# Kernel optimization log

Hardware: AMD Instinct MI355X
Metric: run time of the kernel (lower is better)

## Reference

```python
import jax, jax.numpy as jnp
import numpy as np

N = 100000
IN_C = 128
HID = 16
HEADS = 8
OUT_C = 64
E = 1600000
NEG_SLOPE = 0.2
EPS = 1e-16


def setup_inputs() -> dict:
    key = jax.random.key(0)
    ks = jax.random.split(key, 12)
    s = lambda k, shape, fan: jax.random.normal(k, shape, jnp.float32) * (1.0 / np.sqrt(fan))
    return {
        "x": jax.random.normal(ks[0], (N, IN_C), jnp.float32),
        "edge_index": jax.random.randint(ks[1], (2, E), 0, N, jnp.int64),
        # conv1 params (heads=8, concat=True)
        "W1": s(ks[2], (IN_C, HEADS * HID), IN_C),
        "a_src1": s(ks[3], (HEADS, HID), HID),
        "a_dst1": s(ks[4], (HEADS, HID), HID),
        "b1": jnp.zeros((HEADS * HID,), jnp.float32),
        # conv2 params (heads=1, concat=False)
        "W2": s(ks[5], (HEADS * HID, OUT_C), HEADS * HID),
        "a_src2": s(ks[6], (1, OUT_C), OUT_C),
        "a_dst2": s(ks[7], (1, OUT_C), OUT_C),
        "b2": jnp.zeros((OUT_C,), jnp.float32),
    }


def gat_conv(x, src, dst, W, a_src, a_dst, bias, concat):
    """PyG-style GATConv: edge softmax over incoming edges + scatter-add."""
    H, C = a_src.shape
    n = x.shape[0]
    h = (x @ W).reshape(n, H, C)                      # [N,H,C]
    asrc = jnp.einsum("nhc,hc->nh", h, a_src)          # [N,H]
    adst = jnp.einsum("nhc,hc->nh", h, a_dst)          # [N,H]
    e = jax.nn.leaky_relu(asrc[src] + adst[dst], NEG_SLOPE)  # [E,H]
    # numerically-stable segment softmax over edges sharing a destination
    m = jax.ops.segment_max(e, dst, num_segments=n)    # [N,H]
    m = jnp.where(jnp.isfinite(m), m, 0.0)
    ex = jnp.exp(e - m[dst])                           # [E,H]
    denom = jax.ops.segment_sum(ex, dst, num_segments=n)  # [N,H]
    alpha = ex / (denom[dst] + EPS)                    # [E,H]
    out = jax.ops.segment_sum(alpha[:, :, None] * h[src], dst, num_segments=n)  # [N,H,C]
    out = out.reshape(n, H * C) if concat else out.mean(axis=1)
    return out + bias


def reference(x, edge_index, W1, a_src1, a_dst1, b1, W2, a_src2, a_dst2, b2):
    n = x.shape[0]
    # PyG GATConv adds self-loops by default
    loop = jnp.arange(n, dtype=edge_index.dtype)
    src = jnp.concatenate([edge_index[0], loop])
    dst = jnp.concatenate([edge_index[1], loop])
    # dropout(p=0.6) is identity at inference
    h = jax.nn.elu(gat_conv(x, src, dst, W1, a_src1, a_dst1, b1, concat=True))
    return gat_conv(h, src, dst, W2, a_src2, a_dst2, b2, concat=False)
```

## Files before the change

kernel.cpp:

```cpp
#include <hip/hip_runtime.h>
#include <hip/hip_bf16.h>
#include <math.h>


typedef __attribute__((ext_vector_type(8))) short short8;
typedef __attribute__((ext_vector_type(4))) float f32x4;

__device__ __forceinline__ float bflo(uint u) { return __uint_as_float(u << 16); }
__device__ __forceinline__ float bfhi(uint u) { return __uint_as_float(u & 0xffff0000u); }
__device__ __forceinline__ float bf1(ushort v) { return __uint_as_float(((uint)v) << 16); }
__device__ __forceinline__ ushort f2bf(float f) {
    uint u = __float_as_uint(f);
    u += 0x7fff + ((u >> 16) & 1);
    return (ushort)(u >> 16);
}
#define LOG2E 1.44269504088896f

#define CSR_CAP 4096

__global__ __launch_bounds__(512) void k_bhist(const int* __restrict__ dst, int e,
                                               int* __restrict__ bcount) {
    __shared__ int h[1024];
    int t = threadIdx.x;
    for (int i = t; i < 1024; i += 512) h[i] = 0;
    __syncthreads();
    int c0 = blockIdx.x * 8192, c1 = min(c0 + 8192, e);
    for (int i = c0 + t; i < c1; i += 512) atomicAdd(&h[dst[i] >> 7], 1);
    __syncthreads();
    for (int i = t; i < 1024; i += 512)
        if (h[i]) atomicAdd(&bcount[i], h[i]);
}

__global__ __launch_bounds__(256) void k_bscan(const int* __restrict__ bcount, int nb, int n,
                                               int* __restrict__ ebase, int* __restrict__ ecur,
                                               int* __restrict__ cbase) {
    __shared__ int ae[1024], be[1024], ac[1024], bc[1024];
    int t = threadIdx.x;
    for (int i = t; i < 1024; i += 256) {
        int v = 0, nn = 0;
        if (i < nb) {
            v = bcount[i];
            nn = min(128, n - (i << 7));
        }
        ae[i] = v;
        ac[i] = v + nn;
    }
    __syncthreads();
    int* pa = ae; int* qa = be; int* pc = ac; int* qc = bc;
    for (int off = 1; off < 1024; off <<= 1) {
        for (int i = t; i < 1024; i += 256) {
            int va = pa[i], vc = pc[i];
            if (i >= off) { va += pa[i - off]; vc += pc[i - off]; }
            qa[i] = va; qc[i] = vc;
        }
        __syncthreads();
        int* tm = pa; pa = qa; qa = tm;
        tm = pc; pc = qc; qc = tm;
    }
    for (int i = t; i < 1024; i += 256) {
        if (i < nb) {
            int ea = (i == 0) ? 0 : pa[i - 1];
            int ca = (i == 0) ? 0 : pc[i - 1];
            ebase[i] = ea; ecur[i] = ea; cbase[i] = ca;
        }
    }
}

__global__ __launch_bounds__(512) void k_part(const int* __restrict__ src,
                                              const int* __restrict__ dst, int e,
                                              int* __restrict__ ecur, int* __restrict__ ebuf) {
    __shared__ int h[1024];
    __shared__ int base[1024];
    int t = threadIdx.x;
    int c0 = blockIdx.x * 8192, c1 = min(c0 + 8192, e);
    for (int i = t; i < 1024; i += 512) h[i] = 0;
    __syncthreads();
    for (int i = c0 + t; i < c1; i += 512) atomicAdd(&h[dst[i] >> 7], 1);
    __syncthreads();
    for (int i = t; i < 1024; i += 512) {
        int c = h[i];
        base[i] = c ? atomicAdd(&ecur[i], c) : 0;
        h[i] = 0;
    }
    __syncthreads();
    for (int i = c0 + t; i < c1; i += 512) {
        int d = dst[i], b = d >> 7;
        int r = atomicAdd(&h[b], 1);
        ebuf[base[b] + r] = (src[i] << 7) | (d & 127);
    }
}

__global__ __launch_bounds__(256) void k_build(const int* __restrict__ ebuf,
                                               const int* __restrict__ bcount,
                                               const int* __restrict__ ebase,
                                               const int* __restrict__ cbase,
                                               int* __restrict__ rowptr,
                                               int* __restrict__ csr, int n, int nb) {
    __shared__ int cnt[128];
    __shared__ int sc[128], sc2[128];
    __shared__ int csr_l[CSR_CAP];
    int b = blockIdx.x, t = threadIdx.x;
    int n0 = b << 7;
    int nn = min(128, n - n0);
    int ec = bcount[b], eb = ebase[b], cb = cbase[b];
    if (t < 128) cnt[t] = 0;
    __syncthreads();
    for (int i = t; i < ec; i += 256) atomicAdd(&cnt[ebuf[eb + i] & 127], 1);
    __syncthreads();
    if (t < 128) sc[t] = (t < nn) ? cnt[t] + 1 : 0;
    __syncthreads();
    int* p = sc; int* q = sc2;
    for (int off = 1; off < 128; off <<= 1) {
        if (t < 128) {
            int v = p[t];
            if (t >= off) v += p[t - off];
            q[t] = v;
        }
        __syncthreads();
        int* tm = p; p = q; q = tm;
    }
    int total = p[127];
    if (total <= CSR_CAP) {
        if (t < nn) {
            int off = (t == 0) ? 0 : p[t - 1];
            rowptr[n0 + t] = cb + off;
            csr_l[off] = n0 + t;
            cnt[t] = off + 1;
        }
        __syncthreads();
        for (int i = t; i < ec; i += 256) {
            int v = ebuf[eb + i];
            int s = atomicAdd(&cnt[v & 127], 1);
            csr_l[s] = v >> 7;
        }
        __syncthreads();
        for (int i = t; i < total; i += 256) csr[cb + i] = csr_l[i];
    } else {
        if (t < nn) {
            int off = (t == 0) ? 0 : p[t - 1];
            rowptr[n0 + t] = cb + off;
            csr[cb + off] = n0 + t;
            cnt[t] = off + 1;
        }
        __syncthreads();
        for (int i = t; i < ec; i += 256) {
            int v = ebuf[eb + i];
            int s = atomicAdd(&cnt[v & 127], 1);
            csr[cb + s] = v >> 7;
        }
    }
    if (b == nb - 1 && t == 0) rowptr[n] = cb + total;
}

template <int COLS, bool XBF16>
__global__ __launch_bounds__(256) void k_gemm_mfma(const void* __restrict__ Xv,
                                                   const float* __restrict__ W,
                                                   ushort* __restrict__ Y, int n) {
    __shared__ ushort As[128][136];
    __shared__ ushort Ws[COLS][136];
    const int t = threadIdx.x;
    const int row0 = blockIdx.x * 128;
    if constexpr (!XBF16) {
        const float* X = (const float*)Xv;
#pragma unroll
        for (int q = 0; q < 16; q++) {
            int idx = t + q * 256;
            int r = idx >> 5, c4 = (idx & 31) * 4;
            float4 xv = make_float4(0.f, 0.f, 0.f, 0.f);
            if (row0 + r < n) xv = *reinterpret_cast<const float4*>(&X[(size_t)(row0 + r) * 128 + c4]);
            ushort4 w4 = make_ushort4(f2bf(xv.x), f2bf(xv.y), f2bf(xv.z), f2bf(xv.w));
            *reinterpret_cast<ushort4*>(&As[r][c4]) = w4;
        }
    } else {
        const ushort* X = (const ushort*)Xv;
#pragma unroll
        for (int q = 0; q < 8; q++) {
            int idx = t + q * 256;
            int r = idx >> 4, c8 = (idx & 15) * 8;
            uint4 v = make_uint4(0u, 0u, 0u, 0u);
            if (row0 + r < n) v = *reinterpret_cast<const uint4*>(&X[(size_t)(row0 + r) * 128 + c8]);
            *reinterpret_cast<uint4*>(&As[r][c8]) = v;
        }
    }
    for (int i = t; i < 128 * COLS; i += 256) {
        int k = i / COLS, nc = i % COLS;
        Ws[nc][k] = f2bf(W[i]);
    }
    __syncthreads();
    const int w = t >> 6, l = t & 63;
    const int lr = l & 15;
    const int lk = (l >> 4) * 8;
    f32x4 acc[2][COLS / 16];
#pragma unroll
    for (int m = 0; m < 2; m++)
#pragma unroll
        for (int nb = 0; nb < COLS / 16; nb++) acc[m][nb] = (f32x4){0.f, 0.f, 0.f, 0.f};
#pragma unroll
    for (int kc = 0; kc < 128; kc += 32) {
        short8 a0 = *reinterpret_cast<const short8*>(&As[w * 32 + lr][kc + lk]);
        short8 a1 = *reinterpret_cast<const short8*>(&As[w * 32 + 16 + lr][kc + lk]);
#pragma unroll
        for (int nb = 0; nb < COLS / 16; nb++) {
            short8 bf = *reinterpret_cast<const short8*>(&Ws[nb * 16 + lr][kc + lk]);
            acc[0][nb] = __builtin_amdgcn_mfma_f32_16x16x32_bf16(a0, bf, acc[0][nb], 0, 0, 0);
            acc[1][nb] = __builtin_amdgcn_mfma_f32_16x16x32_bf16(a1, bf, acc[1][nb], 0, 0, 0);
        }
    }
#pragma unroll
    for (int m = 0; m < 2; m++)
#pragma unroll
        for (int j = 0; j < 4; j++) {
            int r = row0 + w * 32 + m * 16 + (l >> 4) * 4 + j;
            if (r < n) {
#pragma unroll
                for (int nb = 0; nb < COLS / 16; nb++)
                    Y[(size_t)r * COLS + nb * 16 + lr] = f2bf(acc[m][nb][j]);
            }
        }
}

__global__ void k_attn1(const uint* __restrict__ hu, const float* __restrict__ a_src,
                        const float* __restrict__ a_dst, float* __restrict__ asrc,
                        float* __restrict__ adst, int n) {
    int t = blockIdx.x * 256 + threadIdx.x;
    if (t >= n * 8) return;
    int node = t >> 3, hd = t & 7;
    const uint* hp = hu + (size_t)node * 64 + hd * 8;
    float s1 = 0.f, s2 = 0.f;
#pragma unroll
    for (int q = 0; q < 8; q++) {
        uint u = hp[q];
        float v0 = bflo(u), v1 = bfhi(u);
        s1 = fmaf(v0, a_src[hd * 16 + 2 * q], s1);
        s1 = fmaf(v1, a_src[hd * 16 + 2 * q + 1], s1);
        s2 = fmaf(v0, a_dst[hd * 16 + 2 * q], s2);
        s2 = fmaf(v1, a_dst[hd * 16 + 2 * q + 1], s2);
    }
    asrc[t] = s1 * LOG2E;
    adst[t] = s2 * LOG2E;
}
__global__ void k_attn2(const uint* __restrict__ hu, const float* __restrict__ a_src,
                        const float* __restrict__ a_dst, float* __restrict__ asrc,
                        float* __restrict__ adst, int n) {
    int t = blockIdx.x * 256 + threadIdx.x;
    if (t >= n * 8) return;
    int node = t >> 3, j = t & 7;
    const uint* hp = hu + (size_t)node * 32 + j * 4;
    float s1 = 0.f, s2 = 0.f;
#pragma unroll
    for (int q = 0; q < 4; q++) {
        uint u = hp[q];
        float v0 = bflo(u), v1 = bfhi(u);
        s1 = fmaf(v0, a_src[j * 8 + 2 * q], s1);
        s1 = fmaf(v1, a_src[j * 8 + 2 * q + 1], s1);
        s2 = fmaf(v0, a_dst[j * 8 + 2 * q], s2);
        s2 = fmaf(v1, a_dst[j * 8 + 2 * q + 1], s2);
    }
#pragma unroll
    for (int o = 1; o < 8; o <<= 1) {
        s1 += __shfl_xor(s1, o);
        s2 += __shfl_xor(s2, o);
    }
    if (j == 0) { asrc[node] = s1 * LOG2E; adst[node] = s2 * LOG2E; }
}

__global__ __launch_bounds__(256) void k_agg1(
    const uint* __restrict__ hu, const float* __restrict__ asrc,
    const float* __restrict__ adst, const int* __restrict__ rowptr,
    const int* __restrict__ csr, const float* __restrict__ b1,
    uint* __restrict__ x2, int n) {
    __shared__ float P[4][512];
    int wv = threadIdx.x >> 6;
    int wid = (blockIdx.x * 256 + threadIdx.x) >> 6;
    if (wid >= n) return;
    uint lane = threadIdx.x & 63;
    uint hd = lane >> 3;
    uint sl = lane & 7;
    uint c0 = lane * 2;
    float adn = adst[(uint)wid * 8u + hd];
    int beg = rowptr[wid], end = rowptr[wid + 1];
    float s = 0.f, acc0 = 0.f, acc1 = 0.f;
    for (int base = beg; base < end; base += 64) {
        int cnt = min(64, end - base);
        int vidx = ((int)lane < cnt) ? csr[base + lane] : 0;
#pragma unroll
        for (int m = 0; m < 8; m++) {
            int slot = 8 * m + (int)sl;
            int cs = csr[base + min(slot, cnt - 1)];
            float e = asrc[(uint)cs * 8u + hd] + adn;
            e = fmaxf(e, 0.2f * e);
            P[wv][slot * 8 + hd] = exp2f(e);
        }
        asm volatile("s_waitcnt lgkmcnt(0)" ::: "memory");
        int j = 0;
        for (; j + 8 <= cnt; j += 8) {
            uint s0 = __builtin_amdgcn_readlane(vidx, j);
            uint s1 = __builtin_amdgcn_readlane(vidx, j + 1);
            uint s2 = __builtin_amdgcn_readlane(vidx, j + 2);
            uint s3 = __builtin_amdgcn_readlane(vidx, j + 3);
            uint s4 = __builtin_amdgcn_readlane(vidx, j + 4);
            uint s5 = __builtin_amdgcn_readlane(vidx, j + 5);
            uint s6 = __builtin_amdgcn_readlane(vidx, j + 6);
            uint s7 = __builtin_amdgcn_readlane(vidx, j + 7);
            uint u0 = hu[s0 * 64u + lane];
            uint u1 = hu[s1 * 64u + lane];
            uint u2 = hu[s2 * 64u + lane];
            uint u3 = hu[s3 * 64u + lane];
            uint u4 = hu[s4 * 64u + lane];
            uint u5 = hu[s5 * 64u + lane];
            uint u6 = hu[s6 * 64u + lane];
            uint u7 = hu[s7 * 64u + lane];
            float q0 = P[wv][(j + 0) * 8 + hd];
            float q1 = P[wv][(j + 1) * 8 + hd];
            float q2 = P[wv][(j + 2) * 8 + hd];
            float q3 = P[wv][(j + 3) * 8 + hd];
            float q4 = P[wv][(j + 4) * 8 + hd];
            float q5 = P[wv][(j + 5) * 8 + hd];
            float q6 = P[wv][(j + 6) * 8 + hd];
            float q7 = P[wv][(j + 7) * 8 + hd];
            s += ((q0 + q1) + (q2 + q3)) + ((q4 + q5) + (q6 + q7));
            acc0 = fmaf(q0, bflo(u0), fmaf(q1, bflo(u1), acc0));
            acc0 = fmaf(q2, bflo(u2), fmaf(q3, bflo(u3), acc0));
            acc0 = fmaf(q4, bflo(u4), fmaf(q5, bflo(u5), acc0));
            acc0 = fmaf(q6, bflo(u6), fmaf(q7, bflo(u7), acc0));
            acc1 = fmaf(q0, bfhi(u0), fmaf(q1, bfhi(u1), acc1));
            acc1 = fmaf(q2, bfhi(u2), fmaf(q3, bfhi(u3), acc1));
            acc1 = fmaf(q4, bfhi(u4), fmaf(q5, bfhi(u5), acc1));
            acc1 = fmaf(q6, bfhi(u6), fmaf(q7, bfhi(u7), acc1));
        }
        for (; j < cnt; ++j) {
            uint s0 = __builtin_amdgcn_readlane(vidx, j);
            float q0 = P[wv][j * 8 + hd];
            uint u0 = hu[s0 * 64u + lane];
            s += q0;
            acc0 = fmaf(q0, bflo(u0), acc0);
            acc1 = fmaf(q0, bfhi(u0), acc1);
        }
    }
    float inv = 1.f / (s + 1e-16f);
    float o0 = acc0 * inv + b1[c0];
    float o1 = acc1 * inv + b1[c0 + 1];
    o0 = o0 > 0.f ? o0 : (__expf(o0) - 1.f);
    o1 = o1 > 0.f ? o1 : (__expf(o1) - 1.f);
    union { ushort b[2]; uint u; } pk;
    pk.b[0] = f2bf(o0);
    pk.b[1] = f2bf(o1);
    x2[(uint)wid * 64u + lane] = pk.u;
}
__global__ __launch_bounds__(256) void k_agg2(
    const ushort* __restrict__ hb, const float* __restrict__ asrc,
    const float* __restrict__ adst, const int* __restrict__ rowptr,
    const int* __restrict__ csr, const float* __restrict__ b2,
    float* __restrict__ out, int n) {
    __shared__ float P2[4][64];
    int wv = threadIdx.x >> 6;
    int wid = (blockIdx.x * 256 + threadIdx.x) >> 6;
    if (wid >= n) return;
    uint lane = threadIdx.x & 63;
    float adn = adst[wid];
    int beg = rowptr[wid], end = rowptr[wid + 1];
    float s = 0.f, acc = 0.f;
    for (int base = beg; base < end; base += 64) {
        int cnt = min(64, end - base);
        int vidx = csr[base + min((int)lane, cnt - 1)];
        float e = asrc[vidx] + adn;
        e = fmaxf(e, 0.2f * e);
        P2[wv][lane] = ((int)lane < cnt) ? exp2f(e) : 0.f;
        asm volatile("s_waitcnt lgkmcnt(0)" ::: "memory");
        int j = 0;
        for (; j + 8 <= cnt; j += 8) {
            uint s0 = __builtin_amdgcn_readlane(vidx, j);
            uint s1 = __builtin_amdgcn_readlane(vidx, j + 1);
            uint s2 = __builtin_amdgcn_readlane(vidx, j + 2);
            uint s3 = __builtin_amdgcn_readlane(vidx, j + 3);
            uint s4 = __builtin_amdgcn_readlane(vidx, j + 4);
            uint s5 = __builtin_amdgcn_readlane(vidx, j + 5);
            uint s6 = __builtin_amdgcn_readlane(vidx, j + 6);
            uint s7 = __builtin_amdgcn_readlane(vidx, j + 7);
            float h0 = bf1(hb[s0 * 64u + lane]);
            float h1 = bf1(hb[s1 * 64u + lane]);
            float h2 = bf1(hb[s2 * 64u + lane]);
            float h3 = bf1(hb[s3 * 64u + lane]);
            float h4 = bf1(hb[s4 * 64u + lane]);
            float h5 = bf1(hb[s5 * 64u + lane]);
            float h6 = bf1(hb[s6 * 64u + lane]);
            float h7 = bf1(hb[s7 * 64u + lane]);
            float q0 = P2[wv][j + 0];
            float q1 = P2[wv][j + 1];
            float q2 = P2[wv][j + 2];
            float q3 = P2[wv][j + 3];
            float q4 = P2[wv][j + 4];
            float q5 = P2[wv][j + 5];
            float q6 = P2[wv][j + 6];
            float q7 = P2[wv][j + 7];
            s += ((q0 + q1) + (q2 + q3)) + ((q4 + q5) + (q6 + q7));
            acc = fmaf(q0, h0, fmaf(q1, h1, acc));
            acc = fmaf(q2, h2, fmaf(q3, h3, acc));
            acc = fmaf(q4, h4, fmaf(q5, h5, acc));
            acc = fmaf(q6, h6, fmaf(q7, h7, acc));
        }
        for (; j < cnt; ++j) {
            uint s0 = __builtin_amdgcn_readlane(vidx, j);
            float q0 = P2[wv][j];
            float h0 = bf1(hb[s0 * 64u + lane]);
            s += q0;
            acc = fmaf(q0, h0, acc);
        }
    }
    out[(size_t)wid * 64 + lane] = acc / (s + 1e-16f) + b2[lane];
}

extern "C" void kernel_launch(void* const* d_in, const int* in_sizes, int n_in,
                              void* d_out, int out_size, void* d_ws, size_t ws_size,
                              hipStream_t stream) {
    const float* x   = (const float*)d_in[0];
    const int*   ei  = (const int*)d_in[1];
    const float* W1  = (const float*)d_in[2];
    const float* as1 = (const float*)d_in[3];
    const float* ad1 = (const float*)d_in[4];
    const float* b1  = (const float*)d_in[5];
    const float* W2  = (const float*)d_in[6];
    const float* as2 = (const float*)d_in[7];
    const float* ad2 = (const float*)d_in[8];
    const float* b2  = (const float*)d_in[9];
    float* out = (float*)d_out;

    int N = in_sizes[0] / 128;
    int E = in_sizes[1] / 2;
    int TOT = E + N;
    const int* src = ei;
    const int* dst = ei + E;

    char* p = (char*)d_ws;
    auto alloc = [&](size_t bytes) {
        char* r = p;
        p += (bytes + 255) & ~size_t(255);
        return r;
    };
    ushort* h1b  = (ushort*)alloc((size_t)N * 128 * 2);
    ushort* h2b  = (ushort*)alloc((size_t)N * 64 * 2);
    ushort* x2b  = (ushort*)alloc((size_t)N * 128 * 2);
    float* asrc1 = (float*)alloc((size_t)N * 8 * 4);
    float* adst1 = (float*)alloc((size_t)N * 8 * 4);
    float* asrc2 = (float*)alloc((size_t)N * 4);
    float* adst2 = (float*)alloc((size_t)N * 4);
    int* rowptr  = (int*)alloc((size_t)(N + 1) * 4);
    int* csr     = (int*)alloc((size_t)TOT * 4);
    int* ebuf    = (int*)alloc((size_t)E * 4);
    int* bcount  = (int*)alloc(1024 * 4);
    int* ebase   = (int*)alloc(1024 * 4);
    int* ecur    = (int*)alloc(1024 * 4);
    int* cbase   = (int*)alloc(1024 * 4);

    int NB = (N + 127) >> 7;
    int nbp = (E + 8191) / 8192;

    hipMemsetAsync(bcount, 0, 1024 * 4, stream);
    k_bhist<<<nbp, 512, 0, stream>>>(dst, E, bcount);
    k_bscan<<<1, 256, 0, stream>>>(bcount, NB, N, ebase, ecur, cbase);
    k_part<<<nbp, 512, 0, stream>>>(src, dst, E, ecur, ebuf);
    k_build<<<NB, 256, 0, stream>>>(ebuf, bcount, ebase, cbase, rowptr, csr, N, NB);

    int gb = (N + 127) / 128;
    k_gemm_mfma<128, false><<<gb, 256, 0, stream>>>(x, W1, h1b, N);
    k_attn1<<<(N * 8 + 255) / 256, 256, 0, stream>>>((const uint*)h1b, as1, ad1, asrc1, adst1, N);
    k_agg1<<<(N + 3) / 4, 256, 0, stream>>>((const uint*)h1b, asrc1, adst1, rowptr, csr, b1,
                                            (uint*)x2b, N);

    k_gemm_mfma<64, true><<<gb, 256, 0, stream>>>(x2b, W2, h2b, N);
    k_attn2<<<(N * 8 + 255) / 256, 256, 0, stream>>>((const uint*)h2b, as2, ad2, asrc2, adst2, N);
    k_agg2<<<(N + 3) / 4, 256, 0, stream>>>((const ushort*)h2b, asrc2, adst2, rowptr, csr, b2,
                                            out, N);
}
```

Measured before the change: 242.0 us.

## Fuse CSR histogram into first GEMM and bucket scan into attention-logit kernel

Merges the edge-destination histogram with the layer-1 GEMM into one launch, with block ranges split by blockIdx and shared memory unioned. It also merges the single-block bucket scan with the layer-1 attention-logit kernel. This cuts two kernel launches and lets independent preprocessing overlap with the dense work. The agg1 edge-logit loop now iterates only over the occupied groups of 8 slots instead of always 8, skipping exp work for short neighbour lists at the cost of loop overhead. The unioned shared memory is sized for the GEMM, so histogram blocks may get lower occupancy.

```diff
diff --git a/kernel.cpp b/kernel.cpp
--- a/kernel.cpp
+++ b/kernel.cpp
@@ -15,55 +15,129 @@
     return (ushort)(u >> 16);
 }
 #define LOG2E 1.44269504088896f
-
 #define CSR_CAP 4096
 
-__global__ __launch_bounds__(512) void k_bhist(const int* __restrict__ dst, int e,
-                                               int* __restrict__ bcount) {
-    __shared__ int h[1024];
-    int t = threadIdx.x;
-    for (int i = t; i < 1024; i += 512) h[i] = 0;
-    __syncthreads();
-    int c0 = blockIdx.x * 8192, c1 = min(c0 + 8192, e);
-    for (int i = c0 + t; i < c1; i += 512) atomicAdd(&h[dst[i] >> 7], 1);
-    __syncthreads();
-    for (int i = t; i < 1024; i += 512)
-        if (h[i]) atomicAdd(&bcount[i], h[i]);
-}
-
-__global__ __launch_bounds__(256) void k_bscan(const int* __restrict__ bcount, int nb, int n,
-                                               int* __restrict__ ebase, int* __restrict__ ecur,
-                                               int* __restrict__ cbase) {
+__global__ __launch_bounds__(256) void k_gemm1_bhist(
+    const float* __restrict__ X, const float* __restrict__ W,
+    ushort* __restrict__ Y, int n,
+    const int* __restrict__ dst, int e, int* __restrict__ bcount, int nbh) {
+    __shared__ union {
+        struct { ushort As[128][136]; ushort Ws[128][136]; } g;
+        int h[1024];
+    } sm;
+    const int t = threadIdx.x;
+    if ((int)blockIdx.x < nbh) {
+        for (int i = t; i < 1024; i += 256) sm.h[i] = 0;
+        __syncthreads();
+        int c0 = blockIdx.x * 8192, c1 = min(c0 + 8192, e);
+        for (int i = c0 + t; i < c1; i += 256) atomicAdd(&sm.h[dst[i] >> 7], 1);
+        __syncthreads();
+        for (int i = t; i < 1024; i += 256)
+            if (sm.h[i]) atomicAdd(&bcount[i], sm.h[i]);
+        return;
+    }
+    const int row0 = (blockIdx.x - nbh) * 128;
+#pragma unroll
+    for (int q = 0; q < 16; q++) {
+        int idx = t + q * 256;
+        int r = idx >> 5, c4 = (idx & 31) * 4;
+        float4 xv = make_float4(0.f, 0.f, 0.f, 0.f);
+        if (row0 + r < n) xv = *reinterpret_cast<const float4*>(&X[(size_t)(row0 + r) * 128 + c4]);
+        ushort4 w4 = make_ushort4(f2bf(xv.x), f2bf(xv.y), f2bf(xv.z), f2bf(xv.w));
+        *reinterpret_cast<ushort4*>(&sm.g.As[r][c4]) = w4;
+    }
+    for (int i = t; i < 128 * 128; i += 256) {
+        int k = i >> 7, nc = i & 127;
+        sm.g.Ws[nc][k] = f2bf(W[i]);
+    }
+    __syncthreads();
+    const int w = t >> 6, l = t & 63;
+    const int lr = l & 15;
+    const int lk = (l >> 4) * 8;
+    f32x4 acc[2][8];
+#pragma unroll
+    for (int m = 0; m < 2; m++)
+#pragma unroll
+        for (int nb = 0; nb < 8; nb++) acc[m][nb] = (f32x4){0.f, 0.f, 0.f, 0.f};
+#pragma unroll
+    for (int kc = 0; kc < 128; kc += 32) {
+        short8 a0 = *reinterpret_cast<const short8*>(&sm.g.As[w * 32 + lr][kc + lk]);
+        short8 a1 = *reinterpret_cast<const short8*>(&sm.g.As[w * 32 + 16 + lr][kc + lk]);
+#pragma unroll
+        for (int nb = 0; nb < 8; nb++) {
+            short8 bf = *reinterpret_cast<const short8*>(&sm.g.Ws[nb * 16 + lr][kc + lk]);
+            acc[0][nb] = __builtin_amdgcn_mfma_f32_16x16x32_bf16(a0, bf, acc[0][nb], 0, 0, 0);
+            acc[1][nb] = __builtin_amdgcn_mfma_f32_16x16x32_bf16(a1, bf, acc[1][nb], 0, 0, 0);
+        }
+    }
+#pragma unroll
+    for (int m = 0; m < 2; m++)
+#pragma unroll
+        for (int j = 0; j < 4; j++) {
+            int r = row0 + w * 32 + m * 16 + (l >> 4) * 4 + j;
+            if (r < n) {
+#pragma unroll
+                for (int nb = 0; nb < 8; nb++)
+                    Y[(size_t)r * 128 + nb * 16 + lr] = f2bf(acc[m][nb][j]);
+            }
+        }
+}
+
+__global__ __launch_bounds__(256) void k_bscan_attn1(
+    const int* __restrict__ bcount, int nb, int n,
+    int* __restrict__ ebase, int* __restrict__ ecur, int* __restrict__ cbase,
+    const uint* __restrict__ hu, const float* __restrict__ a_src,
+    const float* __restrict__ a_dst, float* __restrict__ asrc,
+    float* __restrict__ adst) {
     __shared__ int ae[1024], be[1024], ac[1024], bc[1024];
     int t = threadIdx.x;
-    for (int i = t; i < 1024; i += 256) {
-        int v = 0, nn = 0;
-        if (i < nb) {
-            v = bcount[i];
-            nn = min(128, n - (i << 7));
-        }
-        ae[i] = v;
-        ac[i] = v + nn;
-    }
-    __syncthreads();
-    int* pa = ae; int* qa = be; int* pc = ac; int* qc = bc;
-    for (int off = 1; off < 1024; off <<= 1) {
+    if (blockIdx.x == 0) {
         for (int i = t; i < 1024; i += 256) {
-            int va = pa[i], vc = pc[i];
-            if (i >= off) { va += pa[i - off]; vc += pc[i - off]; }
-            qa[i] = va; qc[i] = vc;
-        }
-        __syncthreads();
-        int* tm = pa; pa = qa; qa = tm;
-        tm = pc; pc = qc; qc = tm;
-    }
-    for (int i = t; i < 1024; i += 256) {
-        if (i < nb) {
-            int ea = (i == 0) ? 0 : pa[i - 1];
-            int ca = (i == 0) ? 0 : pc[i - 1];
-            ebase[i] = ea; ecur[i] = ea; cbase[i] = ca;
-        }
-    }
+            int v = 0, nn = 0;
+            if (i < nb) {
+                v = bcount[i];
+                nn = min(128, n - (i << 7));
+            }
+            ae[i] = v;
+            ac[i] = v + nn;
+        }
+        __syncthreads();
+        int* pa = ae; int* qa = be; int* pc = ac; int* qc = bc;
+        for (int off = 1; off < 1024; off <<= 1) {
+            for (int i = t; i < 1024; i += 256) {
+                int va = pa[i], vc = pc[i];
+                if (i >= off) { va += pa[i - off]; vc += pc[i - off]; }
+                qa[i] = va; qc[i] = vc;
+            }
+            __syncthreads();
+            int* tm = pa; pa = qa; qa = tm;
+            tm = pc; pc = qc; qc = tm;
+        }
+        for (int i = t; i < 1024; i += 256) {
+            if (i < nb) {
+                int ea = (i == 0) ? 0 : pa[i - 1];
+                int ca = (i == 0) ? 0 : pc[i - 1];
+                ebase[i] = ea; ecur[i] = ea; cbase[i] = ca;
+            }
+        }
+        return;
+    }
+    int tt = (blockIdx.x - 1) * 256 + t;
+    if (tt >= n * 8) return;
+    int node = tt >> 3, hd = tt & 7;
+    const uint* hp = hu + (size_t)node * 64 + hd * 8;
+    float s1 = 0.f, s2 = 0.f;
+#pragma unroll
+    for (int q = 0; q < 8; q++) {
+        uint u = hp[q];
+        float v0 = bflo(u), v1 = bfhi(u);
+        s1 = fmaf(v0, a_src[hd * 16 + 2 * q], s1);
+        s1 = fmaf(v1, a_src[hd * 16 + 2 * q + 1], s1);
+        s2 = fmaf(v0, a_dst[hd * 16 + 2 * q], s2);
+        s2 = fmaf(v1, a_dst[hd * 16 + 2 * q + 1], s2);
+    }
+    asrc[tt] = s1 * LOG2E;
+    adst[tt] = s2 * LOG2E;
 }
 
 __global__ __launch_bounds__(512) void k_part(const int* __restrict__ src,
@@ -152,55 +226,40 @@
     if (b == nb - 1 && t == 0) rowptr[n] = cb + total;
 }
 
-template <int COLS, bool XBF16>
-__global__ __launch_bounds__(256) void k_gemm_mfma(const void* __restrict__ Xv,
-                                                   const float* __restrict__ W,
-                                                   ushort* __restrict__ Y, int n) {
+__global__ __launch_bounds__(256) void k_gemm2(const ushort* __restrict__ X,
+                                               const float* __restrict__ W,
+                                               ushort* __restrict__ Y, int n) {
     __shared__ ushort As[128][136];
-    __shared__ ushort Ws[COLS][136];
+    __shared__ ushort Ws[64][136];
     const int t = threadIdx.x;
     const int row0 = blockIdx.x * 128;
-    if constexpr (!XBF16) {
-        const float* X = (const float*)Xv;
-#pragma unroll
-        for (int q = 0; q < 16; q++) {
-            int idx = t + q * 256;
-            int r = idx >> 5, c4 = (idx & 31) * 4;
-            float4 xv = make_float4(0.f, 0.f, 0.f, 0.f);
-            if (row0 + r < n) xv = *reinterpret_cast<const float4*>(&X[(size_t)(row0 + r) * 128 + c4]);
-            ushort4 w4 = make_ushort4(f2bf(xv.x), f2bf(xv.y), f2bf(xv.z), f2bf(xv.w));
-            *reinterpret_cast<ushort4*>(&As[r][c4]) = w4;
-        }
-    } else {
-        const ushort* X = (const ushort*)Xv;
-#pragma unroll
-        for (int q = 0; q < 8; q++) {
-            int idx = t + q * 256;
-            int r = idx >> 4, c8 = (idx & 15) * 8;
-            uint4 v = make_uint4(0u, 0u, 0u, 0u);
-            if (row0 + r < n) v = *reinterpret_cast<const uint4*>(&X[(size_t)(row0 + r) * 128 + c8]);
-            *reinterpret_cast<uint4*>(&As[r][c8]) = v;
-        }
-    }
-    for (int i = t; i < 128 * COLS; i += 256) {
-        int k = i / COLS, nc = i % COLS;
+#pragma unroll
+    for (int q = 0; q < 8; q++) {
+        int idx = t + q * 256;
+        int r = idx >> 4, c8 = (idx & 15) * 8;
+        uint4 v = make_uint4(0u, 0u, 0u, 0u);
+        if (row0 + r < n) v = *reinterpret_cast<const uint4*>(&X[(size_t)(row0 + r) * 128 + c8]);
+        *reinterpret_cast<uint4*>(&As[r][c8]) = v;
+    }
+    for (int i = t; i < 128 * 64; i += 256) {
+        int k = i >> 6, nc = i & 63;
         Ws[nc][k] = f2bf(W[i]);
     }
     __syncthreads();
     const int w = t >> 6, l = t & 63;
     const int lr = l & 15;
     const int lk = (l >> 4) * 8;
-    f32x4 acc[2][COLS / 16];
+    f32x4 acc[2][4];
 #pragma unroll
     for (int m = 0; m < 2; m++)
 #pragma unroll
-        for (int nb = 0; nb < COLS / 16; nb++) acc[m][nb] = (f32x4){0.f, 0.f, 0.f, 0.f};
+        for (int nb = 0; nb < 4; nb++) acc[m][nb] = (f32x4){0.f, 0.f, 0.f, 0.f};
 #pragma unroll
     for (int kc = 0; kc < 128; kc += 32) {
         short8 a0 = *reinterpret_cast<const short8*>(&As[w * 32 + lr][kc + lk]);
         short8 a1 = *reinterpret_cast<const short8*>(&As[w * 32 + 16 + lr][kc + lk]);
 #pragma unroll
-        for (int nb = 0; nb < COLS / 16; nb++) {
+        for (int nb = 0; nb < 4; nb++) {
             short8 bf = *reinterpret_cast<const short8*>(&Ws[nb * 16 + lr][kc + lk]);
             acc[0][nb] = __builtin_amdgcn_mfma_f32_16x16x32_bf16(a0, bf, acc[0][nb], 0, 0, 0);
             acc[1][nb] = __builtin_amdgcn_mfma_f32_16x16x32_bf16(a1, bf, acc[1][nb], 0, 0, 0);
@@ -213,32 +272,12 @@
             int r = row0 + w * 32 + m * 16 + (l >> 4) * 4 + j;
             if (r < n) {
 #pragma unroll
-                for (int nb = 0; nb < COLS / 16; nb++)
-                    Y[(size_t)r * COLS + nb * 16 + lr] = f2bf(acc[m][nb][j]);
+                for (int nb = 0; nb < 4; nb++)
+                    Y[(size_t)r * 64 + nb * 16 + lr] = f2bf(acc[m][nb][j]);
             }
         }
 }
 
-__global__ void k_attn1(const uint* __restrict__ hu, const float* __restrict__ a_src,
-                        const float* __restrict__ a_dst, float* __restrict__ asrc,
-                        float* __restrict__ adst, int n) {
-    int t = blockIdx.x * 256 + threadIdx.x;
-    if (t >= n * 8) return;
-    int node = t >> 3, hd = t & 7;
-    const uint* hp = hu + (size_t)node * 64 + hd * 8;
-    float s1 = 0.f, s2 = 0.f;
-#pragma unroll
-    for (int q = 0; q < 8; q++) {
-        uint u = hp[q];
-        float v0 = bflo(u), v1 = bfhi(u);
-        s1 = fmaf(v0, a_src[hd * 16 + 2 * q], s1);
-        s1 = fmaf(v1, a_src[hd * 16 + 2 * q + 1], s1);
-        s2 = fmaf(v0, a_dst[hd * 16 + 2 * q], s2);
-        s2 = fmaf(v1, a_dst[hd * 16 + 2 * q + 1], s2);
-    }
-    asrc[t] = s1 * LOG2E;
-    adst[t] = s2 * LOG2E;
-}
 __global__ void k_attn2(const uint* __restrict__ hu, const float* __restrict__ a_src,
                         const float* __restrict__ a_dst, float* __restrict__ asrc,
                         float* __restrict__ adst, int n) {
@@ -283,8 +322,8 @@
     for (int base = beg; base < end; base += 64) {
         int cnt = min(64, end - base);
         int vidx = ((int)lane < cnt) ? csr[base + lane] : 0;
-#pragma unroll
-        for (int m = 0; m < 8; m++) {
+        int mb = (cnt + 7) >> 3;
+        for (int m = 0; m < mb; m++) {
             int slot = 8 * m + (int)sl;
             int cs = csr[base + min(slot, cnt - 1)];
             float e = asrc[(uint)cs * 8u + hd] + adn;
@@ -454,20 +493,17 @@
 
     int NB = (N + 127) >> 7;
     int nbp = (E + 8191) / 8192;
+    int gb = (N + 127) / 128;
 
     hipMemsetAsync(bcount, 0, 1024 * 4, stream);
-    k_bhist<<<nbp, 512, 0, stream>>>(dst, E, bcount);
-    k_bscan<<<1, 256, 0, stream>>>(bcount, NB, N, ebase, ecur, cbase);
+    k_gemm1_bhist<<<nbp + gb, 256, 0, stream>>>(x, W1, h1b, N, dst, E, bcount, nbp);
+    k_bscan_attn1<<<1 + (N * 8 + 255) / 256, 256, 0, stream>>>(
+        bcount, NB, N, ebase, ecur, cbase, (const uint*)h1b, as1, ad1, asrc1, adst1);
     k_part<<<nbp, 512, 0, stream>>>(src, dst, E, ecur, ebuf);
     k_build<<<NB, 256, 0, stream>>>(ebuf, bcount, ebase, cbase, rowptr, csr, N, NB);
-
-    int gb = (N + 127) / 128;
-    k_gemm_mfma<128, false><<<gb, 256, 0, stream>>>(x, W1, h1b, N);
-    k_attn1<<<(N * 8 + 255) / 256, 256, 0, stream>>>((const uint*)h1b, as1, ad1, asrc1, adst1, N);
     k_agg1<<<(N + 3) / 4, 256, 0, stream>>>((const uint*)h1b, asrc1, adst1, rowptr, csr, b1,
                                             (uint*)x2b, N);
-
-    k_gemm_mfma<64, true><<<gb, 256, 0, stream>>>(x2b, W2, h2b, N);
+    k_gemm2<<<gb, 256, 0, stream>>>(x2b, W2, h2b, N);
     k_attn2<<<(N * 8 + 255) / 256, 256, 0, stream>>>((const uint*)h2b, as2, ad2, asrc2, adst2, N);
     k_agg2<<<(N + 3) / 4, 256, 0, stream>>>((const ushort*)h2b, asrc2, adst2, rowptr, csr, b2,
                                             out, N);
```

After: 235.8 us. 2.5% less time.
